# Kernel optimization log

Hardware: AMD Instinct MI355X
Metric: run time of the kernel (lower is better)

## Reference

```python
import jax, jax.numpy as jnp
import numpy as np

N, L, D = 2, 1024, 4544
H, DKV = 71, 64
ROPE_BASE = 10000.0


def _rope_tables(seq_len, head_dim, dtype):
    inv_freq = 1.0 / (ROPE_BASE ** (jnp.arange(0, head_dim, 2, dtype=jnp.float32) / head_dim))
    t = jnp.arange(seq_len, dtype=jnp.float32)
    freqs = jnp.outer(t, inv_freq)               # [L, Dkv/2]
    emb = jnp.concatenate([freqs, freqs], -1)    # [L, Dkv]
    return jnp.cos(emb).astype(dtype), jnp.sin(emb).astype(dtype)


def _apply_rotary(x, cos, sin):
    # x: [..., L, Dkv]; cos/sin: [L, Dkv] broadcast
    left, right = jnp.split(x, 2, axis=-1)
    rotated = jnp.concatenate([-right, left], axis=-1)
    return x * cos + rotated * sin


def setup_inputs() -> dict:
    key = jax.random.key(0)
    k1, k2, k3 = jax.random.split(key, 3)
    hidden_states = jax.random.normal(k1, (N, L, D), dtype=jnp.float32)
    w_qkv = jax.random.normal(k2, (D + 2 * DKV, D), dtype=jnp.float32) * (1.0 / np.sqrt(D))
    w_dense = jax.random.normal(k3, (D, D), dtype=jnp.float32) * (1.0 / np.sqrt(D))
    return {"hidden_states": hidden_states, "w_qkv": w_qkv, "w_dense": w_dense}


def reference(hidden_states, w_qkv, w_dense):
    n, l, d = hidden_states.shape
    # fused QKV projection -> [N, L, H+2, Dkv]
    fused = (hidden_states @ w_qkv.T).reshape(n, l, H + 2, DKV)
    q = fused[:, :, :-2, :]          # [N, L, H, Dkv]
    k = fused[:, :, -2, :]           # [N, L, Dkv] (single MQA kv head)
    v = fused[:, :, -1, :]           # [N, L, Dkv]

    cos, sin = _rope_tables(l, DKV, hidden_states.dtype)
    q = _apply_rotary(q, cos[:, None, :], sin[:, None, :])   # broadcast over heads
    k = _apply_rotary(k, cos, sin)

    scale = 1.0 / np.sqrt(DKV)
    # scores: [N, H, Lq, Lk]; kv head broadcast across all H query heads
    scores = jnp.einsum('nqhd,nkd->nhqk', q, k) * scale
    causal = jnp.tril(jnp.ones((l, l), dtype=bool))
    scores = jnp.where(causal, scores, jnp.finfo(scores.dtype).min)
    attn = jax.nn.softmax(scores, axis=-1)
    out = jnp.einsum('nhqk,nkd->nqhd', attn, v)              # [N, L, H, Dkv]
    out = out.reshape(n, l, H * DKV)
    return out @ w_dense.T
```

## Files before the change

### kernel.cpp

```cpp
#include <hip/hip_runtime.h>

typedef unsigned short u16;
typedef __attribute__((ext_vector_type(8))) short short8;
typedef __attribute__((ext_vector_type(4))) float floatx4;

__device__ __forceinline__ u16 f2bf(float f) {
    union { float f; unsigned int u; } v;
    v.f = f;
    unsigned int u = v.u;
    return (u16)((u + 0x7FFFu + ((u >> 16) & 1u)) >> 16);
}

__device__ __forceinline__ void cvt8_f32_bf16(const float* __restrict__ p, u16* dst) {
    const float4 x = *(const float4*)p;
    const float4 y = *(const float4*)(p + 4);
    short8 s;
    s[0] = (short)f2bf(x.x); s[1] = (short)f2bf(x.y);
    s[2] = (short)f2bf(x.z); s[3] = (short)f2bf(x.w);
    s[4] = (short)f2bf(y.x); s[5] = (short)f2bf(y.y);
    s[6] = (short)f2bf(y.z); s[7] = (short)f2bf(y.w);
    *(short8*)dst = s;
}

__device__ __forceinline__ void gld_lds16(const u16* g, u16* l) {
    __builtin_amdgcn_global_load_lds(
        (const __attribute__((address_space(1))) void*)g,
        (__attribute__((address_space(3))) void*)l,
        16, 0, 0);
}

#define DSR(dst, ptr)                                                          \
    asm volatile("ds_read_b128 %0, %1"                                         \
                 : "=v"(dst)                                                   \
                 : "v"((unsigned)(unsigned long long)(const void*)(ptr)))

__global__ __launch_bounds__(256) void cvt3_kernel(
    const float* __restrict__ a, u16* __restrict__ oa, long na,
    const float* __restrict__ b, u16* __restrict__ ob, long nb,
    const float* __restrict__ c, u16* __restrict__ oc, long nc) {
    const float* in; u16* out; long n;
    if (blockIdx.y == 0)      { in = a; out = oa; n = na; }
    else if (blockIdx.y == 1) { in = b; out = ob; n = nb; }
    else                      { in = c; out = oc; n = nc; }
    const long i = ((long)blockIdx.x * 256 + threadIdx.x) * 8;
    if (i >= n) return;
    cvt8_f32_bf16(in + i, out + i);
}


#define GEMM8P_PROLOGUE()                                                      \
    const int t    = threadIdx.x;                                              \
    const int w    = t >> 6;                                                   \
    const int lane = t & 63;                                                   \
    const int quad = lane >> 4;                                                \
    const int l16  = lane & 15;                                                \
    const int sw   = lane & 7;                                                 \
    const int qq = nwgg >> 3, rr = nwgg & 7;                                   \
    const int xcd = blockIdx.x & 7, idx = blockIdx.x >> 3;                     \
    const int wgid = (xcd < rr ? xcd * (qq + 1)                                \
                               : rr * (qq + 1) + (xcd - rr) * qq) + idx;       \
    const int m0 = (wgid / nt) * 256;                                          \
    const int n0 = (wgid % nt) * 256;                                          \
    const int wm = (w >> 2) * 128;                                             \
    const int wn = (w & 3) * 64;                                               \
    const int trow = t >> 3;                                                   \
    const int scol = ((t & 7) ^ (trow & 7)) * 8;                               \
    const long Kl = K;                                                         \
    const u16* Asrc = A + (long)(m0 + trow) * Kl + scol;                       \
    auto stageA = [&](int jt, int h, int b) {                                  \
        _Pragma("unroll")                                                      \
        for (int i = 0; i < 2; i++) {                                          \
            const u16* src = Asrc + (long)(h * 128 + i * 64) * Kl + (long)jt * 64; \
            u16* dst = &aLds[b][0] + h * 8192 + i * 4096 + t * 8;              \
            gld_lds16(src, dst);                                               \
        }                                                                      \
    };                                                                         \
    auto stageB = [&](int jt, int h, int b) {                                  \
        _Pragma("unroll")                                                      \
        for (int i = 0; i < 2; i++) {                                          \
            int rb = n0 + h * 128 + i * 64 + trow;                             \
            if (rb > N - 1) rb = N - 1;                                        \
            const u16* src = B + (long)rb * Kl + scol + (long)jt * 64;         \
            u16* dst = &bLds[b][0] + h * 8192 + i * 4096 + t * 8;              \
            gld_lds16(src, dst);                                               \
        }                                                                      \
    };                                                                         \
    floatx4 acc[8][4];                                                         \
    const floatx4 zf4 = {0.f, 0.f, 0.f, 0.f};                                  \
    _Pragma("unroll")                                                          \
    for (int i = 0; i < 8; i++)                                                \
        _Pragma("unroll")                                                      \
        for (int j = 0; j < 4; j++) acc[i][j] = zf4;                           \
                          \
    stageA(0, 0, 0); stageA(0, 1, 0);                                          \
    stageB(0, 0, 0); stageB(0, 1, 0);                                          \
    stageB(1, 0, 1); stageB(1, 1, 1);                                          \
    asm volatile("s_waitcnt vmcnt(4)" ::: "memory");                           \
    __builtin_amdgcn_s_barrier();

#define ARD(P, rA, rB)                                                         \
    DSR(rA[0], Ac + (wm + (2 * (P)) * 16 + l16) * 64 + ((quad) ^ sw) * 8);     \
    DSR(rB[0], Ac + (wm + (2 * (P) + 1) * 16 + l16) * 64 + ((quad) ^ sw) * 8); \
    DSR(rA[1], Ac + (wm + (2 * (P)) * 16 + l16) * 64 + ((4 + quad) ^ sw) * 8); \
    DSR(rB[1], Ac + (wm + (2 * (P) + 1) * 16 + l16) * 64 + ((4 + quad) ^ sw) * 8);

#define AMM(P, rA, rB)                                                         \
    __builtin_amdgcn_sched_barrier(0);                                         \
    __builtin_amdgcn_s_setprio(1);                                             \
    _Pragma("unroll")                                                          \
    for (int ks = 0; ks < 2; ks++) {                                           \
        _Pragma("unroll")                                                      \
        for (int ni = 0; ni < 4; ni++) {                                       \
            acc[2 * (P)][ni] = __builtin_amdgcn_mfma_f32_16x16x32_bf16(        \
                rA[ks], bf[ni][ks], acc[2 * (P)][ni], 0, 0, 0);                \
            acc[2 * (P) + 1][ni] = __builtin_amdgcn_mfma_f32_16x16x32_bf16(    \
                rB[ks], bf[ni][ks], acc[2 * (P) + 1][ni], 0, 0, 0);            \
        }                                                                      \
    }                                                                          \
    __builtin_amdgcn_s_setprio(0);                                             \
    __builtin_amdgcn_sched_barrier(0);

#define GEMM8P_KLOOP()                                                         \
    const int JT = K >> 6;                                                     \
    for (int j = 0; j < JT; ++j) {                                             \
        const int cur = j & 1;                                                 \
        const int nb  = cur ^ 1;                                               \
        const int jn1 = (j + 1 < JT) ? j + 1 : JT - 1;                         \
        const int jn2 = (j + 2 < JT) ? j + 2 : JT - 1;                         \
        const u16* Ac = &aLds[cur][0];                                         \
        const u16* Bc = &bLds[cur][0];                                         \
        short8 bf[4][2];                                                       \
        short8 aA0[2], aB0[2], aA1[2], aB1[2];                                 \
        short8 aA2[2], aB2[2], aA3[2], aB3[2];                                 \
        _Pragma("unroll")                                                      \
        for (int ni = 0; ni < 4; ni++)                                         \
            _Pragma("unroll")                                                  \
            for (int ks = 0; ks < 2; ks++)                                     \
                DSR(bf[ni][ks],                                                \
                    Bc + (wn + ni * 16 + l16) * 64 + ((4 * ks + quad) ^ sw) * 8); \
        ARD(0, aA0, aB0)                                                       \
        stageA(jn1, 0, nb);                                                    \
        asm volatile("s_waitcnt lgkmcnt(0)" ::: "memory");                     \
        ARD(1, aA1, aB1)                                                       \
        AMM(0, aA0, aB0)                                                       \
        stageA(jn1, 1, nb);                                                    \
        ARD(2, aA2, aB2)                                                       \
        asm volatile("s_waitcnt lgkmcnt(4)" ::: "memory");                     \
        AMM(1, aA1, aB1)                                                       \
        __builtin_amdgcn_s_barrier();    \
        stageB(jn2, 0, cur);                                                   \
        ARD(3, aA3, aB3)                                                       \
        asm volatile("s_waitcnt lgkmcnt(4)" ::: "memory");                     \
        AMM(2, aA2, aB2)                                                       \
        stageB(jn2, 1, cur);                                                   \
        asm volatile("s_waitcnt lgkmcnt(0)" ::: "memory");                     \
        AMM(3, aA3, aB3)                                                       \
        asm volatile("s_waitcnt vmcnt(4)" ::: "memory");                       \
        __builtin_amdgcn_s_barrier();                            \
    }                                                                          \
    asm volatile("s_waitcnt vmcnt(0)" ::: "memory");

__global__ __launch_bounds__(512, 2) void gemm_qkv_8p(
    const u16* __restrict__ A, const u16* __restrict__ B,
    u16* __restrict__ qb, u16* __restrict__ kb, u16* __restrict__ vt,
    int M, int N, int K, int nt,
    const float* __restrict__ cvt_src, u16* __restrict__ cvt_dst, long cvt_n) {
    __shared__ __align__(16) u16 aLds[2][256 * 64];
    __shared__ __align__(16) u16 bLds[2][256 * 64];
    const int nwgg = (M >> 8) * nt;
    if ((int)blockIdx.x >= nwgg) {
        const long blockbase = (long)((int)blockIdx.x - nwgg) * 16384;
#pragma unroll
        for (int u = 0; u < 4; u++) {
            const long i = blockbase + (long)u * 4096 + (long)threadIdx.x * 8;
            if (i < cvt_n) cvt8_f32_bf16(cvt_src + i, cvt_dst + i);
        }
        return;
    }
    GEMM8P_PROLOGUE()
    GEMM8P_KLOOP()

#pragma unroll
    for (int ni = 0; ni < 4; ni++) {
        const int c = n0 + wn + ni * 16 + l16;
        if (c >= N) continue;
        const int hh = c >> 6;
        const int d  = c & 63;
        float inv = 0.f;
        if (hh < 72) inv = expf((float)(2 * (d & 31)) * (-0.14391156831212787f));
#pragma unroll
        for (int mi = 0; mi < 8; mi++) {
#pragma unroll
            for (int r = 0; r < 4; r++) {
                const int row = m0 + wm + mi * 16 + quad * 4 + r;
                const int tn = row >> 10;
                const int tl = row & 1023;
                float val = acc[mi][ni][r];
                if (hh < 72) {
                    float sv, cv;
                    sincosf((float)tl * inv, &sv, &cv);
                    const float pacc = acc[mi][ni ^ 2][r];
                    val = val * cv + ((d < 32) ? -pacc : pacc) * sv;
                }
                if (hh < 71) {
                    qb[((long)((tn * 71 + hh) * 1024 + tl)) * 64 + d] = f2bf(val * 0.125f);
                } else if (hh == 71) {
                    kb[((long)(tn * 1024 + tl)) * 64 + d] = f2bf(val);
                } else {
                    vt[((long)(tn * 64 + d)) * 1024 + tl] = f2bf(val);
                }
            }
        }
    }
}

__global__ __launch_bounds__(512, 2) void gemm_dense_8p(
    const u16* __restrict__ A, const u16* __restrict__ B,
    float* __restrict__ C, int M, int N, int K, int nt) {
    __shared__ __align__(16) u16 aLds[2][256 * 64];
    __shared__ __align__(16) u16 bLds[2][256 * 64];
    const int nwgg = (M >> 8) * nt;
    GEMM8P_PROLOGUE()
    GEMM8P_KLOOP()

#pragma unroll
    for (int ni = 0; ni < 4; ni++) {
        const int col = n0 + wn + ni * 16 + l16;
        if (col >= N) continue;
#pragma unroll
        for (int mi = 0; mi < 8; mi++) {
#pragma unroll
            for (int r = 0; r < 4; r++) {
                const int row = m0 + wm + mi * 16 + quad * 4 + r;
                C[(long)row * N + col] = acc[mi][ni][r];
            }
        }
    }
}

__global__ __launch_bounds__(256) void attn_kernel2(const u16* __restrict__ qb,
                                                    const u16* __restrict__ kb,
                                                    const u16* __restrict__ vt,
                                                    u16* __restrict__ ao) {
    __shared__ __align__(16) u16 k_lds[2][64 * 72];
    __shared__ __align__(16) u16 v_lds[2][64 * 72];
    __shared__ __align__(16) u16 p_lds[4][16 * 72];
    const int qt2 = blockIdx.x;
    const int h   = blockIdx.y;
    const int n   = blockIdx.z;
    const int t    = threadIdx.x;
    const int w    = t >> 6;
    const int lane = t & 63;
    const int quad = lane >> 4;
    const int l16  = lane & 15;
    const int Q0 = qt2 * 128;

    short8 aq[2][2];
#pragma unroll
    for (int mf = 0; mf < 2; mf++) {
        const u16* qrow = qb +
            ((long)((n * 71 + h) * 1024 + Q0 + 64 * mf + w * 16 + l16)) * 64;
        aq[mf][0] = *(const short8*)(qrow + quad * 8);
        aq[mf][1] = *(const short8*)(qrow + 32 + quad * 8);
    }

    floatx4 o[2][4];
    float lst[2][4];
    const floatx4 zf4 = {0.f, 0.f, 0.f, 0.f};
#pragma unroll
    for (int mf = 0; mf < 2; mf++) {
#pragma unroll
        for (int i = 0; i < 4; i++) { o[mf][i] = zf4; lst[mf][i] = 0.f; }
    }

    const int srow = t >> 2;
    const int scol = (t & 3) * 16;
    const u16* kb_n = kb + (long)n * 1024 * 64;
    const u16* vt_n = vt + (long)n * 64 * 1024;
    u16* pw = p_lds[w];

    const int ktend = 2 * qt2 + 2;

    auto stage = [&](int kt, int b) {
        const u16* krow = kb_n + (long)(kt * 64 + srow) * 64 + scol;
        *(uint4*)(k_lds[b] + srow * 72 + scol)     = *(const uint4*)(krow);
        *(uint4*)(k_lds[b] + srow * 72 + scol + 8) = *(const uint4*)(krow + 8);
        const u16* vrow = vt_n + (long)srow * 1024 + kt * 64 + scol;
        *(uint4*)(v_lds[b] + srow * 72 + scol)     = *(const uint4*)(vrow);
        *(uint4*)(v_lds[b] + srow * 72 + scol + 8) = *(const uint4*)(vrow + 8);
    };

    stage(0, 0);
    for (int kt = 0; kt < ktend; kt++) {
        const int buf = kt & 1;
        __syncthreads();
        if (kt + 1 < ktend) stage(kt + 1, 1 - buf);

#pragma unroll
        for (int mf = 0; mf < 2; mf++) {
            if (mf == 0 && kt == 2 * qt2 + 1) continue;
            floatx4 s[4];
#pragma unroll
            for (int sub = 0; sub < 4; sub++) {
                const short8 b0 = *(const short8*)(k_lds[buf] + (sub * 16 + l16) * 72 + quad * 8);
                const short8 b1 = *(const short8*)(k_lds[buf] + (sub * 16 + l16) * 72 + 32 + quad * 8);
                floatx4 z = zf4;
                z = __builtin_amdgcn_mfma_f32_16x16x32_bf16(aq[mf][0], b0, z, 0, 0, 0);
                z = __builtin_amdgcn_mfma_f32_16x16x32_bf16(aq[mf][1], b1, z, 0, 0, 0);
                s[sub] = z;
            }
            const bool diag = (kt == 2 * qt2 + mf);
            const int rowb = Q0 + 64 * mf + w * 16 + quad * 4;
#pragma unroll
            for (int sub = 0; sub < 4; sub++) {
                const int key = kt * 64 + sub * 16 + l16;
#pragma unroll
                for (int r = 0; r < 4; r++) {
                    float p = __expf(s[sub][r]);
                    if (diag && key > rowb + r) p = 0.f;
                    lst[mf][r] += p;
                    pw[(quad * 4 + r) * 72 + sub * 16 + l16] = f2bf(p);
                }
            }
            const short8 ap0 = *(const short8*)(pw + l16 * 72 + quad * 8);
            const short8 ap1 = *(const short8*)(pw + l16 * 72 + 32 + quad * 8);
#pragma unroll
            for (int dch = 0; dch < 4; dch++) {
                const short8 bv0 = *(const short8*)(v_lds[buf] + (dch * 16 + l16) * 72 + quad * 8);
                const short8 bv1 = *(const short8*)(v_lds[buf] + (dch * 16 + l16) * 72 + 32 + quad * 8);
                o[mf][dch] = __builtin_amdgcn_mfma_f32_16x16x32_bf16(ap0, bv0, o[mf][dch], 0, 0, 0);
                o[mf][dch] = __builtin_amdgcn_mfma_f32_16x16x32_bf16(ap1, bv1, o[mf][dch], 0, 0, 0);
            }
        }
    }

    float lsum[2][4];
#pragma unroll
    for (int mf = 0; mf < 2; mf++) {
#pragma unroll
        for (int r = 0; r < 4; r++) {
            float v = lst[mf][r];
#pragma unroll
            for (int mk = 1; mk < 16; mk <<= 1) v += __shfl_xor(v, mk, 64);
            lsum[mf][r] = v;
        }
    }
#pragma unroll
    for (int mf = 0; mf < 2; mf++) {
#pragma unroll
        for (int dch = 0; dch < 4; dch++) {
#pragma unroll
            for (int r = 0; r < 4; r++) {
                const float val = o[mf][dch][r] / lsum[mf][r];
                const int row = n * 1024 + Q0 + 64 * mf + w * 16 + quad * 4 + r;
                const int col = h * 64 + dch * 16 + l16;
                ao[(long)row * 4544 + col] = f2bf(val);
            }
        }
    }
}

__global__ __launch_bounds__(256) void gemm_qkv_f32(const float* __restrict__ A,
                                                    const float* __restrict__ B,
                                                    u16* __restrict__ qb,
                                                    u16* __restrict__ kb,
                                                    u16* __restrict__ vt,
                                                    int M, int N, int K) {
    __shared__ __align__(16) u16 a_lds[128 * 32];
    __shared__ __align__(16) u16 b_lds[128 * 32];
    const int t    = threadIdx.x;
    const int lane = t & 63;
    const int w    = t >> 6;
    const int quad = lane >> 4;
    const int l16  = lane & 15;
    const int m0 = blockIdx.y * 128;
    const int n0 = blockIdx.x * 128;
    const int wm = (w >> 1) * 64;
    const int wn = (w & 1) * 64;
    const int srow = t >> 2;
    const int scol = (t & 3) * 8;
    const float* Ap0 = A + (long)(m0 + srow) * K + scol;
    const float* Ap1 = A + (long)(m0 + 64 + srow) * K + scol;
    int bn0 = n0 + srow;      if (bn0 >= N) bn0 = N - 1;
    int bn1 = n0 + 64 + srow; if (bn1 >= N) bn1 = N - 1;
    const float* Bp0 = B + (long)bn0 * K + scol;
    const float* Bp1 = B + (long)bn1 * K + scol;
    u16* as0 = a_lds + srow * 32 + scol;
    u16* as1 = a_lds + (64 + srow) * 32 + scol;
    u16* bs0 = b_lds + srow * 32 + scol;
    u16* bs1 = b_lds + (64 + srow) * 32 + scol;
    floatx4 acc[4][4];
    const floatx4 zf4 = {0.f, 0.f, 0.f, 0.f};
#pragma unroll
    for (int i = 0; i < 4; i++)
#pragma unroll
        for (int j = 0; j < 4; j++) acc[i][j] = zf4;
    for (int k0 = 0; k0 < K; k0 += 32) {
        cvt8_f32_bf16(Ap0 + k0, as0);
        cvt8_f32_bf16(Ap1 + k0, as1);
        cvt8_f32_bf16(Bp0 + k0, bs0);
        cvt8_f32_bf16(Bp1 + k0, bs1);
        __syncthreads();
        short8 af[4], bfr[4];
#pragma unroll
        for (int i = 0; i < 4; i++)
            af[i] = *(const short8*)(a_lds + (wm + i * 16 + l16) * 32 + quad * 8);
#pragma unroll
        for (int j = 0; j < 4; j++)
            bfr[j] = *(const short8*)(b_lds + (wn + j * 16 + l16) * 32 + quad * 8);
#pragma unroll
        for (int i = 0; i < 4; i++)
#pragma unroll
            for (int j = 0; j < 4; j++)
                acc[i][j] = __builtin_amdgcn_mfma_f32_16x16x32_bf16(af[i], bfr[j], acc[i][j], 0, 0, 0);
        __syncthreads();
    }
#pragma unroll
    for (int j = 0; j < 4; j++) {
        const int c = n0 + wn + j * 16 + l16;
        if (c >= N) continue;
        const int hh = c >> 6;
        const int d  = c & 63;
        float inv = 0.f;
        if (hh < 72) inv = expf((float)(2 * (d & 31)) * (-0.14391156831212787f));
#pragma unroll
        for (int i = 0; i < 4; i++) {
#pragma unroll
            for (int r = 0; r < 4; r++) {
                const int row = m0 + wm + i * 16 + quad * 4 + r;
                const int tn = row >> 10;
                const int tl = row & 1023;
                float val = acc[i][j][r];
                if (hh < 72) {
                    float sv, cv;
                    sincosf((float)tl * inv, &sv, &cv);
                    const float pacc = acc[i][j ^ 2][r];
                    val = val * cv + ((d < 32) ? -pacc : pacc) * sv;
                }
                if (hh < 71) {
                    qb[((long)((tn * 71 + hh) * 1024 + tl)) * 64 + d] = f2bf(val * 0.125f);
                } else if (hh == 71) {
                    kb[((long)(tn * 1024 + tl)) * 64 + d] = f2bf(val);
                } else {
                    vt[((long)(tn * 64 + d)) * 1024 + tl] = f2bf(val);
                }
            }
        }
    }
}

__global__ __launch_bounds__(256) void gemm_dense_f32(const u16* __restrict__ A,
                                                      const float* __restrict__ B,
                                                      float* __restrict__ C,
                                                      int M, int N, int K) {
    __shared__ __align__(16) u16 a_lds[128 * 32];
    __shared__ __align__(16) u16 b_lds[128 * 32];
    const int t    = threadIdx.x;
    const int lane = t & 63;
    const int w    = t >> 6;
    const int quad = lane >> 4;
    const int l16  = lane & 15;
    const int m0 = blockIdx.y * 128;
    const int n0 = blockIdx.x * 128;
    const int wm = (w >> 1) * 64;
    const int wn = (w & 1) * 64;
    const int srow = t >> 2;
    const int scol = (t & 3) * 8;
    const u16* Ap0 = A + (long)(m0 + srow) * K + scol;
    const u16* Ap1 = A + (long)(m0 + 64 + srow) * K + scol;
    int bn0 = n0 + srow;      if (bn0 >= N) bn0 = N - 1;
    int bn1 = n0 + 64 + srow; if (bn1 >= N) bn1 = N - 1;
    const float* Bp0 = B + (long)bn0 * K + scol;
    const float* Bp1 = B + (long)bn1 * K + scol;
    u16* as0 = a_lds + srow * 32 + scol;
    u16* as1 = a_lds + (64 + srow) * 32 + scol;
    u16* bs0 = b_lds + srow * 32 + scol;
    u16* bs1 = b_lds + (64 + srow) * 32 + scol;
    floatx4 acc[4][4];
    const floatx4 zf4 = {0.f, 0.f, 0.f, 0.f};
#pragma unroll
    for (int i = 0; i < 4; i++)
#pragma unroll
        for (int j = 0; j < 4; j++) acc[i][j] = zf4;
    for (int k0 = 0; k0 < K; k0 += 32) {
        *(uint4*)as0 = *(const uint4*)(Ap0 + k0);
        *(uint4*)as1 = *(const uint4*)(Ap1 + k0);
        cvt8_f32_bf16(Bp0 + k0, bs0);
        cvt8_f32_bf16(Bp1 + k0, bs1);
        __syncthreads();
        short8 af[4], bfr[4];
#pragma unroll
        for (int i = 0; i < 4; i++)
            af[i] = *(const short8*)(a_lds + (wm + i * 16 + l16) * 32 + quad * 8);
#pragma unroll
        for (int j = 0; j < 4; j++)
            bfr[j] = *(const short8*)(b_lds + (wn + j * 16 + l16) * 32 + quad * 8);
#pragma unroll
        for (int i = 0; i < 4; i++)
#pragma unroll
            for (int j = 0; j < 4; j++)
                acc[i][j] = __builtin_amdgcn_mfma_f32_16x16x32_bf16(af[i], bfr[j], acc[i][j], 0, 0, 0);
        __syncthreads();
    }
#pragma unroll
    for (int i = 0; i < 4; i++) {
#pragma unroll
        for (int j = 0; j < 4; j++) {
            const int col = n0 + wn + j * 16 + l16;
            if (col < N) {
#pragma unroll
                for (int r = 0; r < 4; r++) {
                    const int row = m0 + wm + i * 16 + quad * 4 + r;
                    C[(long)row * N + col] = acc[i][j][r];
                }
            }
        }
    }
}

extern "C" void kernel_launch(void* const* d_in, const int* in_sizes, int n_in,
                              void* d_out, int out_size, void* d_ws, size_t ws_size,
                              hipStream_t stream) {
    (void)in_sizes; (void)n_in; (void)out_size;
    const float* hidden  = (const float*)d_in[0];
    const float* w_qkv   = (const float*)d_in[1];
    const float* w_dense = (const float*)d_in[2];
    float* out = (float*)d_out;

    const long N_HID = (long)2048 * 4544;
    const long N_QKV = (long)4672 * 4544;
    const long N_DEN = (long)4544 * 4544;
    const long N_Q   = (long)2 * 71 * 1024 * 64;
    const long N_KV  = (long)2 * 1024 * 64;
    const long N_AO  = (long)2048 * 4544;

    const size_t needA = (size_t)(N_HID + N_QKV + N_DEN + N_Q + 2 * N_KV + N_AO) * 2;

    if (ws_size >= needA) {
        u16* hid_bf  = (u16*)d_ws;
        u16* wqkv_bf = hid_bf + N_HID;
        u16* wden_bf = wqkv_bf + N_QKV;
        u16* qbuf    = wden_bf + N_DEN;
        u16* kbuf    = qbuf + N_Q;
        u16* vtbuf   = kbuf + N_KV;
        u16* aout    = vtbuf + N_KV;

        cvt3_kernel<<<dim3(10366, 2), 256, 0, stream>>>(
            hidden, hid_bf, N_HID, w_qkv, wqkv_bf, N_QKV, w_dense, wden_bf, N_DEN);
        gemm_qkv_8p<<<dim3(8 * 19 + 1261), 512, 0, stream>>>(
            hid_bf, wqkv_bf, qbuf, kbuf, vtbuf,
            2048, 4672, 4544, 19,
            w_dense, wden_bf, N_DEN);
        attn_kernel2<<<dim3(8, 71, 2), 256, 0, stream>>>(qbuf, kbuf, vtbuf, aout);
        gemm_dense_8p<<<dim3(8 * 18), 512, 0, stream>>>(aout, wden_bf, out,
                                                        2048, 4544, 4544, 18);
    } else {
        u16* qbuf  = (u16*)d_ws;
        u16* kbuf  = qbuf + N_Q;
        u16* vtbuf = kbuf + N_KV;
        u16* aout  = vtbuf + N_KV;
        gemm_qkv_f32<<<dim3(37, 16), 256, 0, stream>>>(hidden, w_qkv,
                                                       qbuf, kbuf, vtbuf,
                                                       2048, 4672, 4544);
        attn_kernel2<<<dim3(8, 71, 2), 256, 0, stream>>>(qbuf, kbuf, vtbuf, aout);
        gemm_dense_f32<<<dim3(36, 16), 256, 0, stream>>>(aout, w_dense, out,
                                                         2048, 4544, 4544);
    }
}
```

Measured before the change: 527.8 us.

## Software-pipeline LDS fragment reads across K-loop iterations in QKV GEMM

```diff
diff --git a/kernel.cpp b/kernel.cpp
--- a/kernel.cpp
+++ b/kernel.cpp
@@ -98,65 +98,88 @@
     asm volatile("s_waitcnt vmcnt(4)" ::: "memory");                           \
     __builtin_amdgcn_s_barrier();
 
-#define ARD(P, rA, rB)                                                         \
-    DSR(rA[0], Ac + (wm + (2 * (P)) * 16 + l16) * 64 + ((quad) ^ sw) * 8);     \
-    DSR(rB[0], Ac + (wm + (2 * (P) + 1) * 16 + l16) * 64 + ((quad) ^ sw) * 8); \
-    DSR(rA[1], Ac + (wm + (2 * (P)) * 16 + l16) * 64 + ((4 + quad) ^ sw) * 8); \
-    DSR(rB[1], Ac + (wm + (2 * (P) + 1) * 16 + l16) * 64 + ((4 + quad) ^ sw) * 8);
-
-#define AMM(P, rA, rB)                                                         \
+#define RD_BF0(Bp)                                                             \
+    DSR(bk0[0], (Bp) + (wn + 0 * 16 + l16) * 64 + ((quad) ^ sw) * 8);          \
+    DSR(bk0[1], (Bp) + (wn + 1 * 16 + l16) * 64 + ((quad) ^ sw) * 8);          \
+    DSR(bk0[2], (Bp) + (wn + 2 * 16 + l16) * 64 + ((quad) ^ sw) * 8);          \
+    DSR(bk0[3], (Bp) + (wn + 3 * 16 + l16) * 64 + ((quad) ^ sw) * 8);
+#define RD_BF1(Bp)                                                             \
+    DSR(bk1[0], (Bp) + (wn + 0 * 16 + l16) * 64 + ((4 + quad) ^ sw) * 8);      \
+    DSR(bk1[1], (Bp) + (wn + 1 * 16 + l16) * 64 + ((4 + quad) ^ sw) * 8);      \
+    DSR(bk1[2], (Bp) + (wn + 2 * 16 + l16) * 64 + ((4 + quad) ^ sw) * 8);      \
+    DSR(bk1[3], (Bp) + (wn + 3 * 16 + l16) * 64 + ((4 + quad) ^ sw) * 8);
+
+#define RD_A(P, Ap, rA, rB)                                                    \
+    DSR(rA[0], (Ap) + (wm + (2 * (P)) * 16 + l16) * 64 + ((quad) ^ sw) * 8);   \
+    DSR(rB[0], (Ap) + (wm + (2 * (P) + 1) * 16 + l16) * 64 + ((quad) ^ sw) * 8); \
+    DSR(rA[1], (Ap) + (wm + (2 * (P)) * 16 + l16) * 64 + ((4 + quad) ^ sw) * 8); \
+    DSR(rB[1], (Ap) + (wm + (2 * (P) + 1) * 16 + l16) * 64 + ((4 + quad) ^ sw) * 8);
+
+#define CH(P, ks, rA, rB)                                                      \
     __builtin_amdgcn_sched_barrier(0);                                         \
     __builtin_amdgcn_s_setprio(1);                                             \
     _Pragma("unroll")                                                          \
-    for (int ks = 0; ks < 2; ks++) {                                           \
-        _Pragma("unroll")                                                      \
-        for (int ni = 0; ni < 4; ni++) {                                       \
-            acc[2 * (P)][ni] = __builtin_amdgcn_mfma_f32_16x16x32_bf16(        \
-                rA[ks], bf[ni][ks], acc[2 * (P)][ni], 0, 0, 0);                \
-            acc[2 * (P) + 1][ni] = __builtin_amdgcn_mfma_f32_16x16x32_bf16(    \
-                rB[ks], bf[ni][ks], acc[2 * (P) + 1][ni], 0, 0, 0);            \
-        }                                                                      \
+    for (int ni = 0; ni < 4; ni++) {                                           \
+        acc[2 * (P)][ni] = __builtin_amdgcn_mfma_f32_16x16x32_bf16(            \
+            rA[ks], bk##ks[ni], acc[2 * (P)][ni], 0, 0, 0);                    \
+        acc[2 * (P) + 1][ni] = __builtin_amdgcn_mfma_f32_16x16x32_bf16(        \
+            rB[ks], bk##ks[ni], acc[2 * (P) + 1][ni], 0, 0, 0);                \
     }                                                                          \
     __builtin_amdgcn_s_setprio(0);                                             \
     __builtin_amdgcn_sched_barrier(0);
 
 #define GEMM8P_KLOOP()                                                         \
     const int JT = K >> 6;                                                     \
+    short8 bk0[4], bk1[4];                                                     \
+    short8 aA0[2], aB0[2], aA1[2], aB1[2];                                     \
+    short8 aA2[2], aB2[2], aA3[2], aB3[2];                                     \
+    {          \
+        const u16* Ac = &aLds[0][0];                                           \
+        const u16* Bc = &bLds[0][0];                                           \
+        RD_BF0(Bc) RD_BF1(Bc)                                                  \
+        RD_A(0, Ac, aA0, aB0)                                                  \
+        RD_A(1, Ac, aA1, aB1)                                                  \
+        asm volatile("s_waitcnt lgkmcnt(4)" ::: "memory");                     \
+        CH(0, 0, aA0, aB0)                                                     \
+        CH(0, 1, aA0, aB0)                                                     \
+    }                                                                          \
     for (int j = 0; j < JT; ++j) {                                             \
-        const int cur = j & 1;                                                 \
-        const int nb  = cur ^ 1;                                               \
+        const int cur = j & 1, nb = cur ^ 1;                                   \
         const int jn1 = (j + 1 < JT) ? j + 1 : JT - 1;                         \
         const int jn2 = (j + 2 < JT) ? j + 2 : JT - 1;                         \
         const u16* Ac = &aLds[cur][0];                                         \
-        const u16* Bc = &bLds[cur][0];                                         \
-        short8 bf[4][2];                                                       \
-        short8 aA0[2], aB0[2], aA1[2], aB1[2];                                 \
-        short8 aA2[2], aB2[2], aA3[2], aB3[2];                                 \
-        _Pragma("unroll")                                                      \
-        for (int ni = 0; ni < 4; ni++)                                         \
-            _Pragma("unroll")                                                  \
-            for (int ks = 0; ks < 2; ks++)                                     \
-                DSR(bf[ni][ks],                                                \
-                    Bc + (wn + ni * 16 + l16) * 64 + ((4 * ks + quad) ^ sw) * 8); \
-        ARD(0, aA0, aB0)                                                       \
+        const u16* An = &aLds[nb][0];                                          \
+        const u16* Bn = &bLds[nb][0];                                          \
+        RD_A(2, Ac, aA2, aB2)                                                  \
         stageA(jn1, 0, nb);                                                    \
-        asm volatile("s_waitcnt lgkmcnt(0)" ::: "memory");                     \
-        ARD(1, aA1, aB1)                                                       \
-        AMM(0, aA0, aB0)                                                       \
+        asm volatile("s_waitcnt lgkmcnt(4)" ::: "memory");       \
+        CH(1, 0, aA1, aB1)                                                     \
+        CH(1, 1, aA1, aB1)                             \
+        RD_A(3, Ac, aA3, aB3)                                                  \
         stageA(jn1, 1, nb);                                                    \
-        ARD(2, aA2, aB2)                                                       \
-        asm volatile("s_waitcnt lgkmcnt(4)" ::: "memory");                     \
-        AMM(1, aA1, aB1)                                                       \
-        __builtin_amdgcn_s_barrier();    \
+        asm volatile("s_waitcnt lgkmcnt(4)" ::: "memory");       \
+        __builtin_amdgcn_s_barrier();       \
         stageB(jn2, 0, cur);                                                   \
-        ARD(3, aA3, aB3)                                                       \
-        asm volatile("s_waitcnt lgkmcnt(4)" ::: "memory");                     \
-        AMM(2, aA2, aB2)                                                       \
+        CH(2, 0, aA2, aB2)                                                     \
+        CH(2, 1, aA2, aB2)                             \
         stageB(jn2, 1, cur);                                                   \
-        asm volatile("s_waitcnt lgkmcnt(0)" ::: "memory");                     \
-        AMM(3, aA3, aB3)                                                       \
+        asm volatile("s_waitcnt lgkmcnt(0)" ::: "memory");       \
+        CH(3, 0, aA3, aB3)                                       \
         asm volatile("s_waitcnt vmcnt(4)" ::: "memory");                       \
-        __builtin_amdgcn_s_barrier();                            \
+        __builtin_amdgcn_s_barrier();          \
+        if (j + 1 < JT) {                                                      \
+            RD_BF0(Bn)                                                         \
+            RD_A(0, An, aA0, aB0)                                              \
+        }                                                                      \
+        CH(3, 1, aA3, aB3)                      \
+        if (j + 1 < JT) {                                                      \
+            asm volatile("s_waitcnt lgkmcnt(0)" ::: "memory");                 \
+            RD_BF1(Bn)                                                         \
+            RD_A(1, An, aA1, aB1)                                              \
+            CH(0, 0, aA0, aB0)            \
+            asm volatile("s_waitcnt lgkmcnt(4)" ::: "memory");                 \
+            CH(0, 1, aA0, aB0)            \
+        }                                                                      \
     }                                                                          \
     asm volatile("s_waitcnt vmcnt(0)" ::: "memory");
 
```

Result: faster. 502.7 us (-4.7%).
